# Optimization experiments

Hardware: AMD Instinct MI355X
Metric: run time of the kernel (lower is better)

## Reference

```python
import jax, jax.numpy as jnp
import numpy as np

NEG = -1e6  # masked_softmax fill value from the original code


def setup_inputs() -> dict:
    key = jax.random.key(0)
    ks = jax.random.split(key, 8)
    B, Q, K, Dq, Dk, Dv, H = 8, 256, 1024, 256, 256, 128, 128
    queries = jax.random.normal(ks[0], (B, Q, Dq), dtype=jnp.float32)
    keys = jax.random.normal(ks[1], (B, K, Dk), dtype=jnp.float32)
    values = jax.random.normal(ks[2], (B, K, Dv), dtype=jnp.float32)
    valid_lens = jax.random.randint(ks[3], (B,), 1, K + 1, dtype=jnp.int32)
    # learned params (Dense, use_bias=False): y = x @ W
    W_q = jax.random.normal(ks[4], (Dq, H), dtype=jnp.float32) / np.sqrt(Dq)
    W_k = jax.random.normal(ks[5], (Dk, H), dtype=jnp.float32) / np.sqrt(Dk)
    w_v = jax.random.normal(ks[6], (H,), dtype=jnp.float32) / np.sqrt(H)
    return {"queries": queries, "keys": keys, "values": values,
            "valid_lens": valid_lens, "W_q": W_q, "W_k": W_k, "w_v": w_v}


def reference(queries, keys, values, valid_lens, W_q, W_k, w_v):
    q = jnp.einsum('bqd,dh->bqh', queries, W_q)          # [B,Q,H]
    k = jnp.einsum('bkd,dh->bkh', keys, W_k)             # [B,K,H]
    features = jnp.tanh(q[:, :, None, :] + k[:, None, :, :])  # [B,Q,K,H]
    scores = jnp.einsum('bqkh,h->bqk', features, w_v)    # [B,Q,K]
    # masked softmax over last axis: positions >= valid_len set to -1e6
    K_len = scores.shape[-1]
    mask = jnp.arange(K_len)[None, None, :] < valid_lens[:, None, None]
    scores = jnp.where(mask, scores, NEG)
    attn = jax.nn.softmax(scores, axis=-1)
    return jnp.einsum('bqk,bkv->bqv', attn, values)      # [B,Q,Dv]
```

## Files before the change

### kernel.cpp

```cpp
#include <hip/hip_runtime.h>
#include <hip/hip_bf16.h>

#if defined(__has_builtin)
#if __has_builtin(__builtin_amdgcn_exp2f)
#define EXP2F __builtin_amdgcn_exp2f
#endif
#if __has_builtin(__builtin_amdgcn_rcpf)
#define RCPF __builtin_amdgcn_rcpf
#endif
#endif
#ifndef EXP2F
#define EXP2F exp2f
#endif
#ifndef RCPF
#define RCPF(x) (1.0f / (x))
#endif

#define B_  8
#define Q_  256
#define K_  1024
#define D_  256
#define H_  128
#define DV_ 128

#define CSL 2.8853900817779268f
#define L2E 1.4426950408889634f

#define QE_OFF   0
#define KE_OFF   262144
#define WPK_OFF  1310720

__global__ __launch_bounds__(256) void proj_kernel(
    const float* __restrict__ queries, const float* __restrict__ keys,
    const float* __restrict__ Wq, const float* __restrict__ Wk,
    const float* __restrict__ w_v,
    float* __restrict__ qE, float2* __restrict__ kET2, float* __restrict__ wpk)
{
    __shared__ __align__(16) float As[64][68];
    __shared__ __align__(16) float Ws[64][128];

    const int tid = threadIdx.x;
    const int blk = blockIdx.x;
    const bool isQ = blk < 32;
    const int row0 = isQ ? blk * 64 : (blk - 32) * 64;
    const float* A = isQ ? (queries + row0 * D_) : (keys + row0 * D_);
    const float* W = isQ ? Wq : Wk;

    float acc[4][8];
#pragma unroll
    for (int i = 0; i < 4; i++)
#pragma unroll
        for (int j = 0; j < 8; j++) acc[i][j] = 0.f;

    const int lr  = tid & 63;
    const int ldb = (tid >> 6) * 16;
    const int r4  = (tid >> 4) * 4;
    const int c8  = (tid & 15) * 8;

    for (int d0 = 0; d0 < D_; d0 += 64) {
#pragma unroll
        for (int j = 0; j < 4; j++) {
            const float4 a = *(const float4*)&A[lr * D_ + d0 + ldb + j * 4];
            As[ldb + j * 4 + 0][lr] = a.x;
            As[ldb + j * 4 + 1][lr] = a.y;
            As[ldb + j * 4 + 2][lr] = a.z;
            As[ldb + j * 4 + 3][lr] = a.w;
        }
#pragma unroll
        for (int l = 0; l < 8; l++) {
            const int idx = tid + l * 256;
            const int rr = idx >> 5, cc = (idx & 31) * 4;
            *(float4*)&Ws[rr][cc] = *(const float4*)&W[(d0 + rr) * H_ + cc];
        }
        __syncthreads();
#pragma unroll 4
        for (int d = 0; d < 64; d++) {
            const float4 a4 = *(const float4*)&As[d][r4];
            const float4 w0 = *(const float4*)&Ws[d][c8];
            const float4 w1 = *(const float4*)&Ws[d][c8 + 4];
            const float ar[4] = {a4.x, a4.y, a4.z, a4.w};
#pragma unroll
            for (int i = 0; i < 4; i++) {
                acc[i][0] = fmaf(ar[i], w0.x, acc[i][0]);
                acc[i][1] = fmaf(ar[i], w0.y, acc[i][1]);
                acc[i][2] = fmaf(ar[i], w0.z, acc[i][2]);
                acc[i][3] = fmaf(ar[i], w0.w, acc[i][3]);
                acc[i][4] = fmaf(ar[i], w1.x, acc[i][4]);
                acc[i][5] = fmaf(ar[i], w1.y, acc[i][5]);
                acc[i][6] = fmaf(ar[i], w1.z, acc[i][6]);
                acc[i][7] = fmaf(ar[i], w1.w, acc[i][7]);
            }
        }
        __syncthreads();
    }

#pragma unroll
    for (int i = 0; i < 4; i++) {
        float e[8];
#pragma unroll
        for (int j = 0; j < 8; j++) e[j] = EXP2F(CSL * acc[i][j]);
        const int row = row0 + r4 + i;
        if (isQ) {
            float* dst = qE + row * H_ + c8;
            *(float4*)dst = make_float4(e[0], e[1], e[2], e[3]);
            *(float4*)(dst + 4) = make_float4(e[4], e[5], e[6], e[7]);
        } else {
            const int b = row >> 10, k = row & 1023;
            float2* dst = kET2 + (size_t)(b * 64 + (c8 >> 1)) * K_ + k;
#pragma unroll
            for (int jj = 0; jj < 4; jj++)
                dst[jj * K_] = make_float2(e[2 * jj], e[2 * jj + 1]);
        }
    }

    if (blk == 0 && tid < 64) {
        const float w1 = -2.0f * L2E * w_v[2 * tid];
        const float w2 = -2.0f * L2E * w_v[2 * tid + 1];
        *(float4*)&wpk[tid * 4] = make_float4(w1, w2, w1 + w2, 0.f);
    }
}

__global__ __launch_bounds__(1024, 8) void attn_kernel(
    const float* __restrict__ qE,
    const float2* __restrict__ kET2,
    const float* __restrict__ values,
    const int*   __restrict__ valid_lens,
    const float* __restrict__ wpk,
    float* __restrict__ out)
{
    __shared__ __align__(16) float sc[K_][4];
    __shared__ __align__(16) float red[16][4][128];
    __shared__ __align__(16) float psum[16][4];
    __shared__ float rl[4];

    const int tid = threadIdx.x;
    const int b  = blockIdx.y;
    const int q0 = blockIdx.x * 4;
    const int vl = valid_lens[b];

    const float* q0p = qE + (b * Q_ + q0) * H_;
    const float* q1p = q0p + H_;
    const float* q2p = q0p + 2 * H_;
    const float* q3p = q0p + 3 * H_;
    const float2* kb2 = kET2 + (size_t)(b * 64) * K_ + tid;

    float2 acc01 = make_float2(0.f, 0.f);
    float2 acc23 = make_float2(0.f, 0.f);

    if (tid < vl) {
#pragma unroll 4
        for (int p = 0; p < 64; p++) {
            const float2 ek = kb2[(size_t)p * K_];
            const float4 wp = *(const float4*)&wpk[p * 4];
            const float2 qa = *(const float2*)&q0p[2 * p];
            const float2 qb = *(const float2*)&q1p[2 * p];
            const float2 qc = *(const float2*)&q2p[2 * p];
            const float2 qd = *(const float2*)&q3p[2 * p];
            {
                float2 x1 = make_float2(qa.x * ek.x, qb.x * ek.x);
                float2 x2 = make_float2(qa.y * ek.y, qb.y * ek.y);
                float2 e1 = make_float2(x1.x + 1.f, x1.y + 1.f);
                float2 d  = make_float2(fmaf(e1.x, x2.x, e1.x), fmaf(e1.y, x2.y, e1.y));
                float2 n  = make_float2(fmaf(wp.y, x1.x, wp.z), fmaf(wp.y, x1.y, wp.z));
                n = make_float2(fmaf(wp.x, x2.x, n.x), fmaf(wp.x, x2.y, n.y));
                acc01.x = fmaf(n.x, RCPF(d.x), acc01.x);
                acc01.y = fmaf(n.y, RCPF(d.y), acc01.y);
            }
            {
                float2 x1 = make_float2(qc.x * ek.x, qd.x * ek.x);
                float2 x2 = make_float2(qc.y * ek.y, qd.y * ek.y);
                float2 e1 = make_float2(x1.x + 1.f, x1.y + 1.f);
                float2 d  = make_float2(fmaf(e1.x, x2.x, e1.x), fmaf(e1.y, x2.y, e1.y));
                float2 n  = make_float2(fmaf(wp.y, x1.x, wp.z), fmaf(wp.y, x1.y, wp.z));
                n = make_float2(fmaf(wp.x, x2.x, n.x), fmaf(wp.x, x2.y, n.y));
                acc23.x = fmaf(n.x, RCPF(d.x), acc23.x);
                acc23.y = fmaf(n.y, RCPF(d.y), acc23.y);
            }
        }
    }

    const bool valid = tid < vl;
    float4 pv;
    pv.x = valid ? EXP2F(acc01.x) : 0.f;
    pv.y = valid ? EXP2F(acc01.y) : 0.f;
    pv.z = valid ? EXP2F(acc23.x) : 0.f;
    pv.w = valid ? EXP2F(acc23.y) : 0.f;
    *(float4*)&sc[tid][0] = pv;

    float4 s = pv;
#pragma unroll
    for (int sh = 32; sh > 0; sh >>= 1) {
        s.x += __shfl_xor(s.x, sh);
        s.y += __shfl_xor(s.y, sh);
        s.z += __shfl_xor(s.z, sh);
        s.w += __shfl_xor(s.w, sh);
    }
    const int lane = tid & 63, w = tid >> 6;
    if (lane == 0) *(float4*)&psum[w][0] = s;
    __syncthreads();
    if (tid < 4) {
        float t = 0.f;
#pragma unroll
        for (int ww = 0; ww < 16; ww++) t += psum[ww][tid];
        rl[tid] = RCPF(t);
    }

    const int vg = (tid & 31) * 4;
    const int kh = (tid >> 5) & 1;
    const int kc = tid >> 6;
    const float* vb = values + (size_t)b * (K_ * DV_) + vg;
    float av[4][4];
#pragma unroll
    for (int q = 0; q < 4; q++)
#pragma unroll
        for (int j = 0; j < 4; j++) av[q][j] = 0.f;

    const int rem = vl - kc * 64 - kh;
    const int imax = rem <= 0 ? 0 : (((rem + 1) >> 1) > 32 ? 32 : ((rem + 1) >> 1));
#pragma unroll 2
    for (int i = 0; i < imax; i++) {
        const int k = kc * 64 + i * 2 + kh;
        const float4 vv = *(const float4*)&vb[k * DV_];
        const float4 p = *(const float4*)&sc[k][0];
        av[0][0] = fmaf(p.x, vv.x, av[0][0]); av[0][1] = fmaf(p.x, vv.y, av[0][1]);
        av[0][2] = fmaf(p.x, vv.z, av[0][2]); av[0][3] = fmaf(p.x, vv.w, av[0][3]);
        av[1][0] = fmaf(p.y, vv.x, av[1][0]); av[1][1] = fmaf(p.y, vv.y, av[1][1]);
        av[1][2] = fmaf(p.y, vv.z, av[1][2]); av[1][3] = fmaf(p.y, vv.w, av[1][3]);
        av[2][0] = fmaf(p.z, vv.x, av[2][0]); av[2][1] = fmaf(p.z, vv.y, av[2][1]);
        av[2][2] = fmaf(p.z, vv.z, av[2][2]); av[2][3] = fmaf(p.z, vv.w, av[2][3]);
        av[3][0] = fmaf(p.w, vv.x, av[3][0]); av[3][1] = fmaf(p.w, vv.y, av[3][1]);
        av[3][2] = fmaf(p.w, vv.z, av[3][2]); av[3][3] = fmaf(p.w, vv.w, av[3][3]);
    }
#pragma unroll
    for (int q = 0; q < 4; q++)
#pragma unroll
        for (int j = 0; j < 4; j++) av[q][j] += __shfl_xor(av[q][j], 32);
    if (kh == 0) {
#pragma unroll
        for (int q = 0; q < 4; q++)
            *(float4*)&red[kc][q][vg] = make_float4(av[q][0], av[q][1], av[q][2], av[q][3]);
    }
    __syncthreads();

    if (tid < 512) {
        const int q = tid >> 7, v = tid & 127;
        float t = 0.f;
#pragma unroll
        for (int g = 0; g < 16; g++) t += red[g][q][v];
        out[(b * Q_ + q0 + q) * DV_ + v] = t * rl[q];
    }
}

extern "C" void kernel_launch(void* const* d_in, const int* in_sizes, int n_in,
                              void* d_out, int out_size, void* d_ws, size_t ws_size,
                              hipStream_t stream) {
    const float* queries    = (const float*)d_in[0];
    const float* keys       = (const float*)d_in[1];
    const float* values     = (const float*)d_in[2];
    const int*   valid_lens = (const int*)d_in[3];
    const float* W_q        = (const float*)d_in[4];
    const float* W_k        = (const float*)d_in[5];
    const float* w_v        = (const float*)d_in[6];
    float* out = (float*)d_out;

    float*  ws   = (float*)d_ws;
    float*  qE   = ws + QE_OFF;
    float2* kET2 = (float2*)(ws + KE_OFF);
    float*  wpk  = ws + WPK_OFF;

    proj_kernel<<<160, 256, 0, stream>>>(queries, keys, W_q, W_k, w_v, qE, kET2, wpk);
    attn_kernel<<<dim3(Q_ / 4, B_), 1024, 0, stream>>>(qE, kET2, values, valid_lens, wpk, out);
}
```

Baseline: 121.4 us.

## Split projection over column halves and rebalance attention blocks to 2 queries

The projection kernel now splits each 64-row tile into two 64-column halves, doubling the grid to 320 blocks. The attention kernel drops to 512 threads per block handling 2 queries, with each thread computing two keys via float4 loads. Its grid is flattened to 1024 blocks with batch in the low bits. The aim is more blocks for better CU occupancy and load balance across varying valid lengths, at the cost of reloading the key tensor twice as often per query.

```diff
diff --git a/kernel.cpp b/kernel.cpp
--- a/kernel.cpp
+++ b/kernel.cpp
@@ -37,25 +37,28 @@
     float* __restrict__ qE, float2* __restrict__ kET2, float* __restrict__ wpk)
 {
     __shared__ __align__(16) float As[64][68];
-    __shared__ __align__(16) float Ws[64][128];
+    __shared__ __align__(16) float Ws[64][64];
 
     const int tid = threadIdx.x;
     const int blk = blockIdx.x;
-    const bool isQ = blk < 32;
-    const int row0 = isQ ? blk * 64 : (blk - 32) * 64;
+    const bool isQ = blk < 64;
+    const int t = isQ ? blk : (blk - 64);
+    const int rowtile = t >> 1;
+    const int cbase = (t & 1) * 64;
+    const int row0 = rowtile * 64;
     const float* A = isQ ? (queries + row0 * D_) : (keys + row0 * D_);
     const float* W = isQ ? Wq : Wk;
 
-    float acc[4][8];
+    float acc[4][4];
 #pragma unroll
     for (int i = 0; i < 4; i++)
 #pragma unroll
-        for (int j = 0; j < 8; j++) acc[i][j] = 0.f;
+        for (int j = 0; j < 4; j++) acc[i][j] = 0.f;
 
     const int lr  = tid & 63;
     const int ldb = (tid >> 6) * 16;
     const int r4  = (tid >> 4) * 4;
-    const int c8  = (tid & 15) * 8;
+    const int c4  = (tid & 15) * 4;
 
     for (int d0 = 0; d0 < D_; d0 += 64) {
 #pragma unroll
@@ -67,28 +70,23 @@
             As[ldb + j * 4 + 3][lr] = a.w;
         }
 #pragma unroll
-        for (int l = 0; l < 8; l++) {
+        for (int l = 0; l < 4; l++) {
             const int idx = tid + l * 256;
-            const int rr = idx >> 5, cc = (idx & 31) * 4;
-            *(float4*)&Ws[rr][cc] = *(const float4*)&W[(d0 + rr) * H_ + cc];
+            const int rr = idx >> 4, cc = (idx & 15) * 4;
+            *(float4*)&Ws[rr][cc] = *(const float4*)&W[(d0 + rr) * H_ + cbase + cc];
         }
         __syncthreads();
 #pragma unroll 4
         for (int d = 0; d < 64; d++) {
             const float4 a4 = *(const float4*)&As[d][r4];
-            const float4 w0 = *(const float4*)&Ws[d][c8];
-            const float4 w1 = *(const float4*)&Ws[d][c8 + 4];
+            const float4 w4 = *(const float4*)&Ws[d][c4];
             const float ar[4] = {a4.x, a4.y, a4.z, a4.w};
 #pragma unroll
             for (int i = 0; i < 4; i++) {
-                acc[i][0] = fmaf(ar[i], w0.x, acc[i][0]);
-                acc[i][1] = fmaf(ar[i], w0.y, acc[i][1]);
-                acc[i][2] = fmaf(ar[i], w0.z, acc[i][2]);
-                acc[i][3] = fmaf(ar[i], w0.w, acc[i][3]);
-                acc[i][4] = fmaf(ar[i], w1.x, acc[i][4]);
-                acc[i][5] = fmaf(ar[i], w1.y, acc[i][5]);
-                acc[i][6] = fmaf(ar[i], w1.z, acc[i][6]);
-                acc[i][7] = fmaf(ar[i], w1.w, acc[i][7]);
+                acc[i][0] = fmaf(ar[i], w4.x, acc[i][0]);
+                acc[i][1] = fmaf(ar[i], w4.y, acc[i][1]);
+                acc[i][2] = fmaf(ar[i], w4.z, acc[i][2]);
+                acc[i][3] = fmaf(ar[i], w4.w, acc[i][3]);
             }
         }
         __syncthreads();
@@ -96,20 +94,17 @@
 
 #pragma unroll
     for (int i = 0; i < 4; i++) {
-        float e[8];
-#pragma unroll
-        for (int j = 0; j < 8; j++) e[j] = EXP2F(CSL * acc[i][j]);
+        float e[4];
+#pragma unroll
+        for (int j = 0; j < 4; j++) e[j] = EXP2F(CSL * acc[i][j]);
         const int row = row0 + r4 + i;
         if (isQ) {
-            float* dst = qE + row * H_ + c8;
-            *(float4*)dst = make_float4(e[0], e[1], e[2], e[3]);
-            *(float4*)(dst + 4) = make_float4(e[4], e[5], e[6], e[7]);
+            *(float4*)&qE[row * H_ + cbase + c4] = make_float4(e[0], e[1], e[2], e[3]);
         } else {
             const int b = row >> 10, k = row & 1023;
-            float2* dst = kET2 + (size_t)(b * 64 + (c8 >> 1)) * K_ + k;
-#pragma unroll
-            for (int jj = 0; jj < 4; jj++)
-                dst[jj * K_] = make_float2(e[2 * jj], e[2 * jj + 1]);
+            const int p0 = (cbase + c4) >> 1;
+            kET2[(size_t)(b * 64 + p0) * K_ + k]     = make_float2(e[0], e[1]);
+            kET2[(size_t)(b * 64 + p0 + 1) * K_ + k] = make_float2(e[2], e[3]);
         }
     }
 
@@ -120,7 +115,7 @@
     }
 }
 
-__global__ __launch_bounds__(1024, 8) void attn_kernel(
+__global__ __launch_bounds__(512, 8) void attn_kernel(
     const float* __restrict__ qE,
     const float2* __restrict__ kET2,
     const float* __restrict__ values,
@@ -128,126 +123,108 @@
     const float* __restrict__ wpk,
     float* __restrict__ out)
 {
-    __shared__ __align__(16) float sc[K_][4];
-    __shared__ __align__(16) float red[16][4][128];
-    __shared__ __align__(16) float psum[16][4];
-    __shared__ float rl[4];
+    __shared__ __align__(16) float sc[K_][2];
+    __shared__ __align__(16) float red[16][2][128];
+    __shared__ __align__(16) float psum[8][2];
+    __shared__ float rl[2];
 
     const int tid = threadIdx.x;
-    const int b  = blockIdx.y;
-    const int q0 = blockIdx.x * 4;
+    const int b  = blockIdx.x & 7;
+    const int q0 = (blockIdx.x >> 3) * 2;
     const int vl = valid_lens[b];
 
     const float* q0p = qE + (b * Q_ + q0) * H_;
     const float* q1p = q0p + H_;
-    const float* q2p = q0p + 2 * H_;
-    const float* q3p = q0p + 3 * H_;
-    const float2* kb2 = kET2 + (size_t)(b * 64) * K_ + tid;
-
-    float2 acc01 = make_float2(0.f, 0.f);
-    float2 acc23 = make_float2(0.f, 0.f);
-
-    if (tid < vl) {
+    const int k0 = tid * 2;
+
+    float ac00 = 0.f, ac01 = 0.f, ac10 = 0.f, ac11 = 0.f;
+
+    if (k0 < vl) {
+        const float4* kp = (const float4*)kET2 + (size_t)(b * 64) * 512 + tid;
 #pragma unroll 4
         for (int p = 0; p < 64; p++) {
-            const float2 ek = kb2[(size_t)p * K_];
+            const float4 v  = kp[(size_t)p * 512];
             const float4 wp = *(const float4*)&wpk[p * 4];
             const float2 qa = *(const float2*)&q0p[2 * p];
             const float2 qb = *(const float2*)&q1p[2 * p];
-            const float2 qc = *(const float2*)&q2p[2 * p];
-            const float2 qd = *(const float2*)&q3p[2 * p];
             {
-                float2 x1 = make_float2(qa.x * ek.x, qb.x * ek.x);
-                float2 x2 = make_float2(qa.y * ek.y, qb.y * ek.y);
-                float2 e1 = make_float2(x1.x + 1.f, x1.y + 1.f);
-                float2 d  = make_float2(fmaf(e1.x, x2.x, e1.x), fmaf(e1.y, x2.y, e1.y));
-                float2 n  = make_float2(fmaf(wp.y, x1.x, wp.z), fmaf(wp.y, x1.y, wp.z));
-                n = make_float2(fmaf(wp.x, x2.x, n.x), fmaf(wp.x, x2.y, n.y));
-                acc01.x = fmaf(n.x, RCPF(d.x), acc01.x);
-                acc01.y = fmaf(n.y, RCPF(d.y), acc01.y);
+                const float x10 = qa.x * v.x, x20 = qa.y * v.y;
+                const float x11 = qa.x * v.z, x21 = qa.y * v.w;
+                const float e0 = x10 + 1.f, e1 = x11 + 1.f;
+                const float d0 = fmaf(e0, x20, e0), d1 = fmaf(e1, x21, e1);
+                float n0 = fmaf(wp.y, x10, wp.z); n0 = fmaf(wp.x, x20, n0);
+                float n1 = fmaf(wp.y, x11, wp.z); n1 = fmaf(wp.x, x21, n1);
+                ac00 = fmaf(n0, RCPF(d0), ac00);
+                ac01 = fmaf(n1, RCPF(d1), ac01);
             }
             {
-                float2 x1 = make_float2(qc.x * ek.x, qd.x * ek.x);
-                float2 x2 = make_float2(qc.y * ek.y, qd.y * ek.y);
-                float2 e1 = make_float2(x1.x + 1.f, x1.y + 1.f);
-                float2 d  = make_float2(fmaf(e1.x, x2.x, e1.x), fmaf(e1.y, x2.y, e1.y));
-                float2 n  = make_float2(fmaf(wp.y, x1.x, wp.z), fmaf(wp.y, x1.y, wp.z));
-                n = make_float2(fmaf(wp.x, x2.x, n.x), fmaf(wp.x, x2.y, n.y));
-                acc23.x = fmaf(n.x, RCPF(d.x), acc23.x);
-                acc23.y = fmaf(n.y, RCPF(d.y), acc23.y);
+                const float x10 = qb.x * v.x, x20 = qb.y * v.y;
+                const float x11 = qb.x * v.z, x21 = qb.y * v.w;
+                const float e0 = x10 + 1.f, e1 = x11 + 1.f;
+                const float d0 = fmaf(e0, x20, e0), d1 = fmaf(e1, x21, e1);
+                float n0 = fmaf(wp.y, x10, wp.z); n0 = fmaf(wp.x, x20, n0);
+                float n1 = fmaf(wp.y, x11, wp.z); n1 = fmaf(wp.x, x21, n1);
+                ac10 = fmaf(n0, RCPF(d0), ac10);
+                ac11 = fmaf(n1, RCPF(d1), ac11);
             }
         }
     }
 
-    const bool valid = tid < vl;
-    float4 pv;
-    pv.x = valid ? EXP2F(acc01.x) : 0.f;
-    pv.y = valid ? EXP2F(acc01.y) : 0.f;
-    pv.z = valid ? EXP2F(acc23.x) : 0.f;
-    pv.w = valid ? EXP2F(acc23.y) : 0.f;
-    *(float4*)&sc[tid][0] = pv;
-
-    float4 s = pv;
+    const bool v0 = k0 < vl, v1 = (k0 + 1) < vl;
+    const float p00 = v0 ? EXP2F(ac00) : 0.f;
+    const float p10 = v0 ? EXP2F(ac10) : 0.f;
+    const float p01 = v1 ? EXP2F(ac01) : 0.f;
+    const float p11 = v1 ? EXP2F(ac11) : 0.f;
+    *(float4*)&sc[k0][0] = make_float4(p00, p10, p01, p11);
+
+    float s0 = p00 + p01, s1 = p10 + p11;
 #pragma unroll
     for (int sh = 32; sh > 0; sh >>= 1) {
-        s.x += __shfl_xor(s.x, sh);
-        s.y += __shfl_xor(s.y, sh);
-        s.z += __shfl_xor(s.z, sh);
-        s.w += __shfl_xor(s.w, sh);
+        s0 += __shfl_xor(s0, sh);
+        s1 += __shfl_xor(s1, sh);
     }
     const int lane = tid & 63, w = tid >> 6;
-    if (lane == 0) *(float4*)&psum[w][0] = s;
+    if (lane == 0) { psum[w][0] = s0; psum[w][1] = s1; }
     __syncthreads();
-    if (tid < 4) {
-        float t = 0.f;
-#pragma unroll
-        for (int ww = 0; ww < 16; ww++) t += psum[ww][tid];
-        rl[tid] = RCPF(t);
+    if (tid < 2) {
+        float tsum = 0.f;
+#pragma unroll
+        for (int ww = 0; ww < 8; ww++) tsum += psum[ww][tid];
+        rl[tid] = RCPF(tsum);
     }
 
     const int vg = (tid & 31) * 4;
-    const int kh = (tid >> 5) & 1;
-    const int kc = tid >> 6;
+    const int kc = tid >> 5;
     const float* vb = values + (size_t)b * (K_ * DV_) + vg;
-    float av[4][4];
-#pragma unroll
-    for (int q = 0; q < 4; q++)
+    float av[2][4];
+#pragma unroll
+    for (int q = 0; q < 2; q++)
 #pragma unroll
         for (int j = 0; j < 4; j++) av[q][j] = 0.f;
 
-    const int rem = vl - kc * 64 - kh;
-    const int imax = rem <= 0 ? 0 : (((rem + 1) >> 1) > 32 ? 32 : ((rem + 1) >> 1));
+    const int rem = vl - kc * 64;
+    const int imax = rem <= 0 ? 0 : (rem > 64 ? 64 : rem);
 #pragma unroll 2
     for (int i = 0; i < imax; i++) {
-        const int k = kc * 64 + i * 2 + kh;
+        const int k = kc * 64 + i;
         const float4 vv = *(const float4*)&vb[k * DV_];
-        const float4 p = *(const float4*)&sc[k][0];
-        av[0][0] = fmaf(p.x, vv.x, av[0][0]); av[0][1] = fmaf(p.x, vv.y, av[0][1]);
-        av[0][2] = fmaf(p.x, vv.z, av[0][2]); av[0][3] = fmaf(p.x, vv.w, av[0][3]);
-        av[1][0] = fmaf(p.y, vv.x, av[1][0]); av[1][1] = fmaf(p.y, vv.y, av[1][1]);
-        av[1][2] = fmaf(p.y, vv.z, av[1][2]); av[1][3] = fmaf(p.y, vv.w, av[1][3]);
-        av[2][0] = fmaf(p.z, vv.x, av[2][0]); av[2][1] = fmaf(p.z, vv.y, av[2][1]);
-        av[2][2] = fmaf(p.z, vv.z, av[2][2]); av[2][3] = fmaf(p.z, vv.w, av[2][3]);
-        av[3][0] = fmaf(p.w, vv.x, av[3][0]); av[3][1] = fmaf(p.w, vv.y, av[3][1]);
-        av[3][2] = fmaf(p.w, vv.z, av[3][2]); av[3][3] = fmaf(p.w, vv.w, av[3][3]);
-    }
-#pragma unroll
-    for (int q = 0; q < 4; q++)
-#pragma unroll
-        for (int j = 0; j < 4; j++) av[q][j] += __shfl_xor(av[q][j], 32);
-    if (kh == 0) {
-#pragma unroll
-        for (int q = 0; q < 4; q++)
-            *(float4*)&red[kc][q][vg] = make_float4(av[q][0], av[q][1], av[q][2], av[q][3]);
-    }
+        const float2 pp = *(const float2*)&sc[k][0];
+        av[0][0] = fmaf(pp.x, vv.x, av[0][0]); av[0][1] = fmaf(pp.x, vv.y, av[0][1]);
+        av[0][2] = fmaf(pp.x, vv.z, av[0][2]); av[0][3] = fmaf(pp.x, vv.w, av[0][3]);
+        av[1][0] = fmaf(pp.y, vv.x, av[1][0]); av[1][1] = fmaf(pp.y, vv.y, av[1][1]);
+        av[1][2] = fmaf(pp.y, vv.z, av[1][2]); av[1][3] = fmaf(pp.y, vv.w, av[1][3]);
+    }
+#pragma unroll
+    for (int q = 0; q < 2; q++)
+        *(float4*)&red[kc][q][vg] = make_float4(av[q][0], av[q][1], av[q][2], av[q][3]);
     __syncthreads();
 
-    if (tid < 512) {
+    if (tid < 256) {
         const int q = tid >> 7, v = tid & 127;
-        float t = 0.f;
-#pragma unroll
-        for (int g = 0; g < 16; g++) t += red[g][q][v];
-        out[(b * Q_ + q0 + q) * DV_ + v] = t * rl[q];
+        float tsum = 0.f;
+#pragma unroll
+        for (int g = 0; g < 16; g++) tsum += red[g][q][v];
+        out[(b * Q_ + q0 + q) * DV_ + v] = tsum * rl[q];
     }
 }
 
@@ -268,6 +245,6 @@
     float2* kET2 = (float2*)(ws + KE_OFF);
     float*  wpk  = ws + WPK_OFF;
 
-    proj_kernel<<<160, 256, 0, stream>>>(queries, keys, W_q, W_k, w_v, qE, kET2, wpk);
-    attn_kernel<<<dim3(Q_ / 4, B_), 1024, 0, stream>>>(qE, kET2, values, valid_lens, wpk, out);
+    proj_kernel<<<320, 256, 0, stream>>>(queries, keys, W_q, W_k, w_v, qE, kET2, wpk);
+    attn_kernel<<<1024, 512, 0, stream>>>(qE, kET2, values, valid_lens, wpk, out);
 }
```

Result: slower. 127.8 us (+5.3%).
